# Performance work log

Hardware: AMD Instinct MI355X
Metric: run time of the kernel (lower is better)

Reference implementation:

```python
import jax, jax.numpy as jnp
import numpy as np

B, S, D = 4, 4096, 2048
DECAY_BIAS_INIT = -4.0
W_SCALE = 0.02


def setup_inputs() -> dict:
    key = jax.random.key(0)
    ks = jax.random.split(key, 6)
    return {
        "x": jax.random.normal(ks[0], (B, S, D), dtype=jnp.float32),
        "W_in": jax.random.normal(ks[1], (D, D), dtype=jnp.float32) * W_SCALE,
        "b_in": jnp.zeros((D,), jnp.float32),
        "W_decay": jax.random.normal(ks[2], (D, D), dtype=jnp.float32) * W_SCALE,
        "b_decay": jnp.zeros((D,), jnp.float32),
        "W_gate": jax.random.normal(ks[3], (D, D), dtype=jnp.float32) * W_SCALE,
        "b_gate": jnp.zeros((D,), jnp.float32),
        "W_out": jax.random.normal(ks[4], (D, D), dtype=jnp.float32) * W_SCALE,
        "b_out": jnp.zeros((D,), jnp.float32),
        "decay_bias": jnp.full((D,), DECAY_BIAS_INIT, jnp.float32),
    }


def reference(x, W_in, b_in, W_decay, b_decay, W_gate, b_gate, W_out, b_out, decay_bias):
    # Projections (weights stored as [in, out]; torch Linear applies x @ W.T, here W is pre-transposed)
    inp = jax.nn.silu(jnp.einsum("bsd,de->bse", x, W_in) + b_in).astype(jnp.float32)
    decay = jax.nn.sigmoid(jnp.einsum("bsd,de->bse", x, W_decay) + b_decay + decay_bias)
    gate = jax.nn.sigmoid(jnp.einsum("bsd,de->bse", x, W_gate) + b_gate)

    # Gated linear recurrence: s_t = d_t * s_{t-1} + (1 - d_t) * i_t
    def step(state, di):
        d, i = di
        state = d * state + (1.0 - d) * i
        return state, state

    init = jnp.zeros((x.shape[0], x.shape[2]), jnp.float32)
    _, states = jax.lax.scan(
        step, init, (jnp.swapaxes(decay, 0, 1), jnp.swapaxes(inp, 0, 1))
    )  # states: [S, B, D]
    y = gate * jnp.swapaxes(states, 0, 1)  # [B, S, D]
    y = y.astype(x.dtype)
    return jnp.einsum("bsd,de->bse", y, W_out) + b_out
```

## Files before the change

### kernel.cpp

```cpp
#include <hip/hip_runtime.h>

typedef unsigned short u16;
typedef __attribute__((ext_vector_type(4))) float f4;
typedef __attribute__((ext_vector_type(8))) short s8v;
typedef __attribute__((ext_vector_type(8))) unsigned short u16x8;
typedef __attribute__((ext_vector_type(4))) unsigned short u16x4;

#define B_   4
#define S_   4096
#define D_   2048
#define M_   (B_ * S_)
#define K_   D_
#define N3_  (3 * D_)
#define CCH  128
#define LCH  32
#define NTK  32

__device__ __forceinline__ u16 f2bf(float f) {
  unsigned u = __float_as_uint(f);
  u += 0x7FFF + ((u >> 16) & 1);
  return (u16)(u >> 16);
}
__device__ __forceinline__ float bf2f(u16 h) {
  return __uint_as_float(((unsigned)h) << 16);
}
__device__ __forceinline__ float sigm(float z) {
  return 1.0f / (1.0f + __expf(-z));
}

__global__ void k_cvt(const float* __restrict__ src, u16* __restrict__ dst, int n4) {
  int i = blockIdx.x * 256 + threadIdx.x;
  if (i >= n4) return;
  f4 v = *(const f4*)(src + (size_t)i * 4);
  u16x4 o;
  o[0] = f2bf(v[0]); o[1] = f2bf(v[1]); o[2] = f2bf(v[2]); o[3] = f2bf(v[3]);
  *(u16x4*)(dst + (size_t)i * 4) = o;
}

__global__ void k_tcvt(const float* __restrict__ src, u16* __restrict__ dst) {
  __shared__ float tile[32][33];
  int tx = threadIdx.x & 31, ty = threadIdx.x >> 5;
  int c0 = blockIdx.x * 32, r0 = blockIdx.y * 32;
#pragma unroll
  for (int j = 0; j < 32; j += 8)
    tile[ty + j][tx] = src[(size_t)(r0 + ty + j) * 2048 + c0 + tx];
  __syncthreads();
#pragma unroll
  for (int j = 0; j < 32; j += 8)
    dst[(size_t)(c0 + ty + j) * 2048 + r0 + tx] = f2bf(tile[tx][ty + j]);
}

__global__ void __launch_bounds__(512, 2)
k_gemm256(const u16* __restrict__ A, const u16* __restrict__ BT, int N, int mode,
          u16* __restrict__ o_inp, u16* __restrict__ o_dec, u16* __restrict__ o_gate,
          const float* __restrict__ b_in, const float* __restrict__ b_dec,
          const float* __restrict__ b_gate, const float* __restrict__ dbias,
          float* __restrict__ o_f, const float* __restrict__ b_out) {
  extern __shared__ u16 smem[];
  u16* const Asb[2] = { smem,         smem + 16384 };
  u16* const Bsb[2] = { smem + 32768, smem + 49152 };

  const int ntn = N >> 8;
  const int nwg = gridDim.x;
  const int bid = blockIdx.x;
  const int wg = (bid & 7) * (nwg >> 3) + (bid >> 3);
  const int tile_m = (wg / ntn) << 8;
  const int tile_n = (wg % ntn) << 8;
  const int tid = threadIdx.x;
  const int wave = tid >> 6, lane = tid & 63;
  const int wm = (wave >> 2) << 7;
  const int wn = (wave & 3) << 6;
  const int l15 = lane & 15, lhi = lane >> 4;
  const int srow = tid >> 3, sslot = tid & 7;

  f4 acc[8][4];
#pragma unroll
  for (int m = 0; m < 8; ++m)
#pragma unroll
    for (int n = 0; n < 4; ++n)
#pragma unroll
      for (int r = 0; r < 4; ++r) acc[m][n][r] = 0.0f;

  s8v bfr[2][4];

  auto STAGE = [&](const u16* __restrict__ G, int grow0, u16* L, int c, int k0) {
    int r = (c << 6) + srow;
    int sc = (sslot ^ (r & 7)) << 3;
    __builtin_amdgcn_global_load_lds(
        (const __attribute__((address_space(1))) unsigned int*)(G + (size_t)(grow0 + r) * K_ + k0 + sc),
        (__attribute__((address_space(3))) unsigned int*)(L + (((c << 6) + (wave << 3)) << 6)),
        16, 0, 0);
  };

#pragma unroll
  for (int c = 0; c < 4; ++c) STAGE(A, tile_m, Asb[0], c, 0);
#pragma unroll
  for (int c = 0; c < 4; ++c) STAGE(BT, tile_n, Bsb[0], c, 0);
#pragma unroll
  for (int c = 0; c < 4; ++c) STAGE(BT, tile_n, Bsb[1], c, 64);
  STAGE(A, tile_m, Asb[1], 0, 64);
  STAGE(A, tile_m, Asb[1], 2, 64);
  asm volatile("s_waitcnt vmcnt(6)" ::: "memory");
  __builtin_amdgcn_s_barrier();

  for (int it = 0; it < NTK / 2; ++it) {
    const int t0 = it << 1;
#pragma unroll
    for (int p = 0; p < 8; ++p) {
      const int toff[8] = {1, 2, 2, 2, 2, 3, 3, 3};
      const int sopA[8] = {1, 0, 0, 1, 1, 0, 0, 1};
      const int sc0[8]  = {1, 0, 2, 0, 1, 0, 2, 0};
      const int sc1f[8] = {3, 1, 3, 2, 3, 1, 3, 2};
      const int q = p & 3;
      u16* const Acur = Asb[p >> 2];
      u16* const Bcur = Bsb[p >> 2];

      s8v afr[2][2];
#pragma unroll
      for (int kk = 0; kk < 2; ++kk)
#pragma unroll
        for (int mi = 0; mi < 2; ++mi) {
          int r = wm + ((q * 2 + mi) << 4) + l15;
          afr[mi][kk] = *(const s8v*)(Acur + (r << 6) + ((((kk << 2) + lhi) ^ (r & 7)) << 3));
        }
      if (q == 0) {
#pragma unroll
        for (int kk = 0; kk < 2; ++kk)
#pragma unroll
          for (int n = 0; n < 4; ++n) {
            int r = wn + (n << 4) + l15;
            bfr[kk][n] = *(const s8v*)(Bcur + (r << 6) + ((((kk << 2) + lhi) ^ (r & 7)) << 3));
          }
      }

      {
        const int st = (t0 + toff[p]) & (NTK - 1);
        const int k0s = st << 6;
        u16* const Ad = Asb[st & 1];
        u16* const Bd = Bsb[st & 1];
        if (sopA[p]) { STAGE(A, tile_m, Ad, sc0[p], k0s); STAGE(A, tile_m, Ad, sc1f[p], k0s); }
        else         { STAGE(BT, tile_n, Bd, sc0[p], k0s); STAGE(BT, tile_n, Bd, sc1f[p], k0s); }
      }
      if (q == 3) {
        asm volatile("s_waitcnt vmcnt(6)" ::: "memory");
        __builtin_amdgcn_sched_barrier(0);
      }
      __builtin_amdgcn_s_barrier();

      __builtin_amdgcn_s_setprio(1);
#pragma unroll
      for (int kk = 0; kk < 2; ++kk)
#pragma unroll
        for (int mi = 0; mi < 2; ++mi)
#pragma unroll
          for (int n = 0; n < 4; ++n)
            acc[q * 2 + mi][n] =
                __builtin_amdgcn_mfma_f32_16x16x32_bf16(afr[mi][kk], bfr[kk][n], acc[q * 2 + mi][n], 0, 0, 0);
      __builtin_amdgcn_s_setprio(0);
      __builtin_amdgcn_s_barrier();
    }
  }

  asm volatile("s_waitcnt vmcnt(0)" ::: "memory");
  __builtin_amdgcn_s_barrier();

  if (mode == 0) {
    const int selb = tile_n >> 11;
    const int dbase = tile_n & 2047;
    float bias[4];
#pragma unroll
    for (int n = 0; n < 4; ++n) {
      int d = dbase + wn + (n << 4) + l15;
      bias[n] = (selb == 0) ? b_in[d] : (selb == 1) ? (b_dec[d] + dbias[d]) : b_gate[d];
    }
#pragma unroll
    for (int m = 0; m < 8; ++m)
#pragma unroll
      for (int n = 0; n < 4; ++n)
#pragma unroll
        for (int r = 0; r < 4; ++r) {
          int lrow = wm + (m << 4) + (lhi << 2) + r;
          int lcol = wn + (n << 4) + l15;
          float z = acc[m][n][r] + bias[n];
          float v = (selb == 0) ? z * sigm(z) : sigm(z);
          smem[(lrow << 8) + (((lcol >> 3) ^ (lrow & 7)) << 3) + (lcol & 7)] = f2bf(v);
        }
    __builtin_amdgcn_s_barrier();
    u16* const dst = (selb == 0) ? o_inp : (selb == 1) ? o_dec : o_gate;
    const int rr = tid >> 5, sl = tid & 31;
#pragma unroll
    for (int pass = 0; pass < 16; ++pass) {
      int row = (pass << 4) + rr;
      u16x8 v = *(const u16x8*)(smem + (row << 8) + ((sl ^ (row & 7)) << 3));
      *(u16x8*)(dst + (size_t)(tile_m + row) * D_ + dbase + (sl << 3)) = v;
    }
  } else {
    float* const Tf = (float*)smem;
    f4 bo = *(const f4*)(b_out + tile_n + (lane << 2));
#pragma unroll
    for (int sw = 0; sw < 2; ++sw) {
      if (sw) __builtin_amdgcn_s_barrier();
      if ((wm >> 7) == sw) {
#pragma unroll
        for (int m = 0; m < 8; ++m)
#pragma unroll
          for (int n = 0; n < 4; ++n)
#pragma unroll
            for (int r = 0; r < 4; ++r) {
              int lrow = (m << 4) + (lhi << 2) + r;
              int lcol = wn + (n << 4) + l15;
              Tf[(lrow << 8) + (((lcol >> 2) ^ (lrow & 7)) << 2) + (lcol & 3)] = acc[m][n][r];
            }
      }
      __builtin_amdgcn_s_barrier();
#pragma unroll
      for (int pass = 0; pass < 16; ++pass) {
        int lrow = (pass << 3) + wave;
        f4 v = *(const f4*)(Tf + (lrow << 8) + ((lane ^ (lrow & 7)) << 2));
        v[0] += bo[0]; v[1] += bo[1]; v[2] += bo[2]; v[3] += bo[3];
        *(f4*)(o_f + (size_t)(tile_m + (sw << 7) + lrow) * D_ + tile_n + (lane << 2)) = v;
      }
    }
  }
}

__global__ void k_scan1(const u16* __restrict__ dec, const u16* __restrict__ inp,
                        float* __restrict__ chA, float* __restrict__ chB) {
  int b = blockIdx.x / CCH, c = blockIdx.x % CCH;
  int d0 = threadIdx.x * 8;
  const u16* dp = dec + ((size_t)b * S_ + c * LCH) * D_ + d0;
  const u16* ip = inp + ((size_t)b * S_ + c * LCH) * D_ + d0;
  float Aa[8], st[8];
#pragma unroll
  for (int i = 0; i < 8; ++i) { Aa[i] = 1.0f; st[i] = 0.0f; }
#pragma unroll 4
  for (int j = 0; j < LCH; ++j) {
    u16x8 dv = *(const u16x8*)(dp + (size_t)j * D_);
    u16x8 iv = *(const u16x8*)(ip + (size_t)j * D_);
#pragma unroll
    for (int i = 0; i < 8; ++i) {
      float dd = bf2f(dv[i]), ii = bf2f(iv[i]);
      Aa[i] *= dd;
      st[i] = dd * st[i] + (1.0f - dd) * ii;
    }
  }
  size_t o = ((size_t)b * CCH + c) * D_ + d0;
#pragma unroll
  for (int i = 0; i < 8; ++i) { chA[o + i] = Aa[i]; chB[o + i] = st[i]; }
}

__global__ void k_scan2(const float* __restrict__ chA, const float* __restrict__ chB,
                        float* __restrict__ ini) {
  int b = blockIdx.x >> 3;
  int d = ((blockIdx.x & 7) << 8) + threadIdx.x;
  float st = 0.0f;
  for (int c = 0; c < CCH; ++c) {
    size_t o = ((size_t)b * CCH + c) * D_ + d;
    ini[o] = st;
    st = chA[o] * st + chB[o];
  }
}

__global__ void k_scan3(const u16* __restrict__ dec, const u16* __restrict__ inp,
                        const u16* __restrict__ gat, const float* __restrict__ ini,
                        u16* __restrict__ y) {
  int b = blockIdx.x / CCH, c = blockIdx.x % CCH;
  int d0 = threadIdx.x * 8;
  size_t ib = ((size_t)b * CCH + c) * D_ + d0;
  float st[8];
#pragma unroll
  for (int i = 0; i < 8; ++i) st[i] = ini[ib + i];
  size_t base = ((size_t)b * S_ + c * LCH) * D_ + d0;
#pragma unroll 4
  for (int j = 0; j < LCH; ++j) {
    size_t o = base + (size_t)j * D_;
    u16x8 dv = *(const u16x8*)(dec + o);
    u16x8 iv = *(const u16x8*)(inp + o);
    u16x8 gv = *(const u16x8*)(gat + o);
    u16x8 yv;
#pragma unroll
    for (int i = 0; i < 8; ++i) {
      float dd = bf2f(dv[i]), ii = bf2f(iv[i]);
      st[i] = dd * st[i] + (1.0f - dd) * ii;
      yv[i] = f2bf(bf2f(gv[i]) * st[i]);
    }
    *(u16x8*)(y + o) = yv;
  }
}

extern "C" void kernel_launch(void* const* d_in, const int* in_sizes, int n_in,
                              void* d_out, int out_size, void* d_ws, size_t ws_size,
                              hipStream_t stream) {
  (void)in_sizes; (void)n_in; (void)out_size; (void)ws_size;
  const float* x      = (const float*)d_in[0];
  const float* W_in   = (const float*)d_in[1];
  const float* b_in   = (const float*)d_in[2];
  const float* W_dec  = (const float*)d_in[3];
  const float* b_dec  = (const float*)d_in[4];
  const float* W_gate = (const float*)d_in[5];
  const float* b_gate = (const float*)d_in[6];
  const float* W_out  = (const float*)d_in[7];
  const float* b_out  = (const float*)d_in[8];
  const float* dbias  = (const float*)d_in[9];
  float* out = (float*)d_out;

  char* ws = (char*)d_ws;
  u16*   xb  = (u16*)(ws);
  u16*   w3t = (u16*)(ws + 67108864ull);
  u16*   wot = (u16*)(ws + 92274688ull);
  u16*   inp = (u16*)(ws + 100663296ull);
  u16*   dec = (u16*)(ws + 167772160ull);
  u16*   gat = (u16*)(ws + 234881024ull);
  float* chA = (float*)(ws + 301989888ull);
  float* chB = (float*)(ws + 306184192ull);
  float* ini = (float*)(ws + 310378496ull);
  u16*   y   = xb;

  hipFuncSetAttribute((const void*)k_gemm256,
                      hipFuncAttributeMaxDynamicSharedMemorySize, 131072);

  k_cvt<<<32768, 256, 0, stream>>>(x, xb, 8388608);
  k_tcvt<<<dim3(64, 64), 256, 0, stream>>>(W_in,   w3t);
  k_tcvt<<<dim3(64, 64), 256, 0, stream>>>(W_dec,  w3t + 2048 * 2048);
  k_tcvt<<<dim3(64, 64), 256, 0, stream>>>(W_gate, w3t + 2 * 2048 * 2048);
  k_tcvt<<<dim3(64, 64), 256, 0, stream>>>(W_out,  wot);

  k_gemm256<<<(M_ / 256) * (N3_ / 256), 512, 131072, stream>>>(
      xb, w3t, N3_, 0, inp, dec, gat, b_in, b_dec, b_gate, dbias, nullptr, nullptr);

  k_scan1<<<B_ * CCH, 256, 0, stream>>>(dec, inp, chA, chB);
  k_scan2<<<32, 256, 0, stream>>>(chA, chB, ini);
  k_scan3<<<B_ * CCH, 256, 0, stream>>>(dec, inp, gat, ini, y);

  k_gemm256<<<(M_ / 256) * (D_ / 256), 512, 131072, stream>>>(
      y, wot, D_, 1, nullptr, nullptr, nullptr, nullptr, nullptr, nullptr, nullptr,
      out, b_out);
}
```

Measured before the change: 668.1 us.

## Restructure GEMM main loop into four half-phases and remap tiles per XCD

The main GEMM loop drops the eight-phase table-driven schedule and uses four phases per iteration. Each phase issues a whole 64-wide k-slab of A or B staging and runs 32 MFMAs per wave over half the M fragments, so there are fewer barriers per k-step. Block-to-tile mapping changes so each XCD owns a fixed band of 8 M-tiles and walks 8x8 super-blocks over N, aiming for better L2 reuse. Prefetch depth and waitcnt accounting change, which risks stalls or hazards if the counts are wrong, and the fixed mapping assumes specific grid sizes.

New measurement: 671.5 us. About the same (+0.5%).

```diff
diff --git a/kernel.cpp b/kernel.cpp
--- a/kernel.cpp
+++ b/kernel.cpp
@@ -60,12 +60,14 @@
   u16* const Asb[2] = { smem,         smem + 16384 };
   u16* const Bsb[2] = { smem + 32768, smem + 49152 };
 
-  const int ntn = N >> 8;
-  const int nwg = gridDim.x;
   const int bid = blockIdx.x;
-  const int wg = (bid & 7) * (nwg >> 3) + (bid >> 3);
-  const int tile_m = (wg / ntn) << 8;
-  const int tile_n = (wg % ntn) << 8;
+  const int xcd = bid & 7, j = bid >> 3;
+  const int nsb = j >> 6;
+  const int rj = j & 63;
+  const int mm = rj >> 3, nn = rj & 7;
+  const int tile_m = ((xcd << 3) + mm) << 8;
+  const int tile_n = ((nsb << 3) + nn) << 8;
+
   const int tid = threadIdx.x;
   const int wave = tid >> 6, lane = tid & 63;
   const int wm = (wave >> 2) << 7;
@@ -92,73 +94,87 @@
         16, 0, 0);
   };
 
+  auto RDB = [&](u16* Bb) {
+#pragma unroll
+    for (int kk = 0; kk < 2; ++kk)
+#pragma unroll
+      for (int n = 0; n < 4; ++n) {
+        int r = wn + (n << 4) + l15;
+        bfr[kk][n] = *(const s8v*)(Bb + (r << 6) + ((((kk << 2) + lhi) ^ (r & 7)) << 3));
+      }
+  };
+
+  auto RDMM = [&](u16* Ab, int qbase) {
+    s8v a[2][2][2];
+#pragma unroll
+    for (int kk = 0; kk < 2; ++kk)
+#pragma unroll
+      for (int qi = 0; qi < 2; ++qi)
+#pragma unroll
+        for (int mi = 0; mi < 2; ++mi) {
+          int r = wm + (((qbase + qi) * 2 + mi) << 4) + l15;
+          a[qi][mi][kk] = *(const s8v*)(Ab + (r << 6) + ((((kk << 2) + lhi) ^ (r & 7)) << 3));
+        }
+    __builtin_amdgcn_s_setprio(1);
+#pragma unroll
+    for (int kk = 0; kk < 2; ++kk)
+#pragma unroll
+      for (int qi = 0; qi < 2; ++qi)
+#pragma unroll
+        for (int mi = 0; mi < 2; ++mi)
+#pragma unroll
+          for (int n = 0; n < 4; ++n)
+            acc[(qbase + qi) * 2 + mi][n] =
+                __builtin_amdgcn_mfma_f32_16x16x32_bf16(a[qi][mi][kk], bfr[kk][n],
+                                                        acc[(qbase + qi) * 2 + mi][n], 0, 0, 0);
+    __builtin_amdgcn_s_setprio(0);
+  };
+
 #pragma unroll
   for (int c = 0; c < 4; ++c) STAGE(A, tile_m, Asb[0], c, 0);
 #pragma unroll
   for (int c = 0; c < 4; ++c) STAGE(BT, tile_n, Bsb[0], c, 0);
 #pragma unroll
   for (int c = 0; c < 4; ++c) STAGE(BT, tile_n, Bsb[1], c, 64);
-  STAGE(A, tile_m, Asb[1], 0, 64);
-  STAGE(A, tile_m, Asb[1], 2, 64);
-  asm volatile("s_waitcnt vmcnt(6)" ::: "memory");
+  asm volatile("s_waitcnt vmcnt(4)" ::: "memory");
   __builtin_amdgcn_s_barrier();
 
+#pragma unroll 1
   for (int it = 0; it < NTK / 2; ++it) {
     const int t0 = it << 1;
-#pragma unroll
-    for (int p = 0; p < 8; ++p) {
-      const int toff[8] = {1, 2, 2, 2, 2, 3, 3, 3};
-      const int sopA[8] = {1, 0, 0, 1, 1, 0, 0, 1};
-      const int sc0[8]  = {1, 0, 2, 0, 1, 0, 2, 0};
-      const int sc1f[8] = {3, 1, 3, 2, 3, 1, 3, 2};
-      const int q = p & 3;
-      u16* const Acur = Asb[p >> 2];
-      u16* const Bcur = Bsb[p >> 2];
-
-      s8v afr[2][2];
-#pragma unroll
-      for (int kk = 0; kk < 2; ++kk)
-#pragma unroll
-        for (int mi = 0; mi < 2; ++mi) {
-          int r = wm + ((q * 2 + mi) << 4) + l15;
-          afr[mi][kk] = *(const s8v*)(Acur + (r << 6) + ((((kk << 2) + lhi) ^ (r & 7)) << 3));
-        }
-      if (q == 0) {
-#pragma unroll
-        for (int kk = 0; kk < 2; ++kk)
-#pragma unroll
-          for (int n = 0; n < 4; ++n) {
-            int r = wn + (n << 4) + l15;
-            bfr[kk][n] = *(const s8v*)(Bcur + (r << 6) + ((((kk << 2) + lhi) ^ (r & 7)) << 3));
-          }
-      }
-
-      {
-        const int st = (t0 + toff[p]) & (NTK - 1);
-        const int k0s = st << 6;
-        u16* const Ad = Asb[st & 1];
-        u16* const Bd = Bsb[st & 1];
-        if (sopA[p]) { STAGE(A, tile_m, Ad, sc0[p], k0s); STAGE(A, tile_m, Ad, sc1f[p], k0s); }
-        else         { STAGE(BT, tile_n, Bd, sc0[p], k0s); STAGE(BT, tile_n, Bd, sc1f[p], k0s); }
-      }
-      if (q == 3) {
-        asm volatile("s_waitcnt vmcnt(6)" ::: "memory");
-        __builtin_amdgcn_sched_barrier(0);
-      }
-      __builtin_amdgcn_s_barrier();
-
-      __builtin_amdgcn_s_setprio(1);
-#pragma unroll
-      for (int kk = 0; kk < 2; ++kk)
-#pragma unroll
-        for (int mi = 0; mi < 2; ++mi)
-#pragma unroll
-          for (int n = 0; n < 4; ++n)
-            acc[q * 2 + mi][n] =
-                __builtin_amdgcn_mfma_f32_16x16x32_bf16(afr[mi][kk], bfr[kk][n], acc[q * 2 + mi][n], 0, 0, 0);
-      __builtin_amdgcn_s_setprio(0);
-      __builtin_amdgcn_s_barrier();
-    }
+    const int k1 = ((t0 + 1) & (NTK - 1)) << 6;
+    const int k2 = ((t0 + 2) & (NTK - 1)) << 6;
+    const int k3 = ((t0 + 3) & (NTK - 1)) << 6;
+
+    STAGE(A, tile_m, Asb[1], 0, k1); STAGE(A, tile_m, Asb[1], 2, k1);
+    STAGE(A, tile_m, Asb[1], 1, k1); STAGE(A, tile_m, Asb[1], 3, k1);
+    __builtin_amdgcn_s_barrier();
+    RDB(Bsb[0]);
+    RDMM(Asb[0], 0);
+    __builtin_amdgcn_s_barrier();
+
+    STAGE(BT, tile_n, Bsb[0], 0, k2); STAGE(BT, tile_n, Bsb[0], 1, k2);
+    STAGE(BT, tile_n, Bsb[0], 2, k2); STAGE(BT, tile_n, Bsb[0], 3, k2);
+    asm volatile("s_waitcnt vmcnt(6)" ::: "memory");
+    __builtin_amdgcn_sched_barrier(0);
+    __builtin_amdgcn_s_barrier();
+    RDMM(Asb[0], 2);
+    __builtin_amdgcn_s_barrier();
+
+    STAGE(A, tile_m, Asb[0], 0, k2); STAGE(A, tile_m, Asb[0], 2, k2);
+    STAGE(A, tile_m, Asb[0], 1, k2); STAGE(A, tile_m, Asb[0], 3, k2);
+    __builtin_amdgcn_s_barrier();
+    RDB(Bsb[1]);
+    RDMM(Asb[1], 0);
+    __builtin_amdgcn_s_barrier();
+
+    STAGE(BT, tile_n, Bsb[1], 0, k3); STAGE(BT, tile_n, Bsb[1], 1, k3);
+    STAGE(BT, tile_n, Bsb[1], 2, k3); STAGE(BT, tile_n, Bsb[1], 3, k3);
+    asm volatile("s_waitcnt vmcnt(6)" ::: "memory");
+    __builtin_amdgcn_sched_barrier(0);
+    __builtin_amdgcn_s_barrier();
+    RDMM(Asb[1], 2);
+    __builtin_amdgcn_s_barrier();
   }
 
   asm volatile("s_waitcnt vmcnt(0)" ::: "memory");
```
